# Kernel optimization log

Measured on AMD Instinct MI355X. Metric: run time of the kernel, lower is better.

## Reference

```python
import jax, jax.numpy as jnp
import numpy as np

K = 3          # kernel_size
PAD = 1        # padding
HEADS = 4
C = 128
K2 = K * K


def setup_inputs() -> dict:
    key = jax.random.key(0)
    k1, k2, k3, k4 = jax.random.split(key, 4)
    B, H, W = 4, 128, 128
    x = jax.random.normal(k1, (B, H, W, C), jnp.float32)
    w_qkv = jax.random.normal(k2, (K2 * K2 * HEADS, C), jnp.float32) * 0.02
    w_v = jax.random.normal(k3, (K2, C, C), jnp.float32) * np.sqrt(2.0 / (K2 * C))
    w_proj = jax.random.normal(k4, (C, C), jnp.float32) * 0.02
    return {"x": x, "w_qkv": w_qkv, "w_v": w_v, "w_proj": w_proj}


def _csa(x, w_qkv, w_v, w_proj):
    B, H, W, Cc = x.shape
    hd = Cc // HEADS
    scale = hd ** (-0.5)
    N = H * W
    # attention map: Linear(C -> k^4*heads); pool is identity for stride=1
    att = jnp.einsum('bhwc,oc->bhwo', x, w_qkv)                      # [B,H,W,81*heads]
    att = att.reshape(B, N, HEADS, K2, K2).transpose(0, 2, 1, 3, 4)  # [B,heads,N,k2,k2]
    att = jax.nn.softmax(att * scale, axis=-1)
    # unfold x into per-location 3x3 windows (patch index p = di*K + dj)
    xp = jnp.pad(x, ((0, 0), (PAD, PAD), (PAD, PAD), (0, 0)))
    patches = jnp.stack([xp[:, di:di + H, dj:dj + W, :]
                         for di in range(K) for dj in range(K)], axis=3)  # [B,H,W,k2,C]
    v = patches.reshape(B, N, K2, Cc)
    # grouped 1x1 conv == per-window-position CxC matmul
    v = jnp.einsum('pij,bnpj->bnpi', w_v, v)                          # [B,N,k2,C]
    v = v.reshape(B, N, K2, HEADS, hd).transpose(0, 3, 1, 2, 4)       # [B,heads,N,k2,hd]
    out = jnp.einsum('bhnpq,bhnqd->bhnpd', att, v)                    # [B,heads,N,k2,hd]
    # -> [B, C, k2, H, W] with channel index = head*hd + d (matches torch fold layout)
    out = out.transpose(0, 1, 4, 3, 2).reshape(B, Cc, K2, H, W)
    # fold: scatter-add overlapping patches back to (H, W)
    acc = jnp.zeros((B, Cc, H + 2 * PAD, W + 2 * PAD), x.dtype)
    p = 0
    for di in range(K):
        for dj in range(K):
            acc = acc.at[:, :, di:di + H, dj:dj + W].add(out[:, :, p])
            p += 1
    y = acc[:, :, PAD:PAD + H, PAD:PAD + W].transpose(0, 2, 3, 1)     # [B,H,W,C]
    return jnp.einsum('bhwc,oc->bhwo', y, w_proj)


def reference(x, w_qkv, w_v, w_proj):
    return _csa(x, w_qkv, w_v, w_proj)
```

## Files before the change

kernel.cpp:

```cpp
#include <hip/hip_runtime.h>


typedef short bf16x8 __attribute__((ext_vector_type(8)));
typedef float f32x4  __attribute__((ext_vector_type(4)));
typedef float v2f    __attribute__((ext_vector_type(2)));

#define SCALE 0.17677669529663687f

__device__ __forceinline__ unsigned short f2bf(float f) {
  unsigned u = __float_as_uint(f);
  u = (u + 0x7fffu + ((u >> 16) & 1u)) >> 16;
  return (unsigned short)u;
}
__device__ __forceinline__ float bf2f(unsigned short s) {
  return __uint_as_float(((unsigned)s) << 16);
}
__device__ __forceinline__ unsigned pk2bf(float lo, float hi) {
  unsigned a = __float_as_uint(lo) + 0x8000u;
  unsigned b = __float_as_uint(hi) + 0x8000u;
  return __builtin_amdgcn_perm(b, a, 0x07060302u);
}
__device__ __forceinline__ bf16x8 ld16(const unsigned short* p) {
  union { bf16x8 v; uint4 u; } r;
  r.u = *(const uint4*)p;
  return r.v;
}

__global__ __launch_bounds__(256) void cvt_kernel(const float* __restrict__ wq,
                                                  const float* __restrict__ wv,
                                                  const float* __restrict__ wp,
                                                  unsigned short* __restrict__ wqb,
                                                  unsigned short* __restrict__ wvb2,
                                                  unsigned short* __restrict__ wpb2) {
  int i = blockIdx.x * 256 + threadIdx.x;
  if (i >= 30848) return;
  if (i < 10368) {
    long off = (long)i * 4;
    float4 v = *(const float4*)(wq + off);
    ushort4 o;
    o.x = f2bf(v.x); o.y = f2bf(v.y); o.z = f2bf(v.z); o.w = f2bf(v.w);
    *(ushort4*)(wqb + off) = o;
    return;
  }
  const float* s;
  unsigned short* d;
  if (i < 28800) {
    int it = i - 10368;
    int l = it & 63, mk = it >> 6;
    int kk = mk & 3, m = (mk >> 2) & 1, qcg = mk >> 3;
    int cg = qcg & 3, q = qcg >> 2;
    int chan = cg * 32 + m * 16 + (l & 15);
    int k0 = kk * 32 + (l >> 4) * 8;
    s = wv + (long)q * 16384 + chan * 128 + k0;
    d = wvb2 + (long)it * 8;
  } else {
    int it = i - 28800;
    int l = it & 63, kk = (it >> 6) & 3, tn = it >> 8;
    int col = tn * 16 + (l & 15);
    int k0 = kk * 32 + (l >> 4) * 8;
    s = wp + (long)col * 128 + k0;
    d = wpb2 + (long)it * 8;
  }
  float4 a = *(const float4*)s, b = *(const float4*)(s + 4);
  ushort4 o0, o1;
  o0.x = f2bf(a.x); o0.y = f2bf(a.y); o0.z = f2bf(a.z); o0.w = f2bf(a.w);
  o1.x = f2bf(b.x); o1.y = f2bf(b.y); o1.z = f2bf(b.z); o1.w = f2bf(b.w);
  *(ushort4*)d = o0;
  *(ushort4*)(d + 4) = o1;
}

__device__ __forceinline__ void softmax9(const float* L, unsigned short* attile,
                                         int row, int p) {
  float mx = L[0];
#pragma unroll
  for (int q = 1; q < 9; q++) mx = fmaxf(mx, L[q]);
  float e[9], s = 0.f;
#pragma unroll
  for (int q = 0; q < 9; q++) { e[q] = __expf((L[q] - mx) * SCALE); s += e[q]; }
  float inv = 1.f / s;
#pragma unroll
  for (int q = 0; q < 9; q++) attile[row * 90 + q * 10 + p] = f2bf(e[q] * inv);
}

__global__ __launch_bounds__(512, 6) void att_kernel(const float* __restrict__ x,
                                                     const unsigned short* __restrict__ wqb,
                                                     unsigned* __restrict__ attb) {
  __shared__ unsigned short Bl[96 * 136];
  __shared__ float lg[64][84];
  const int t = threadIdx.x;
  const long m0 = (long)blockIdx.x * 64;
  const int w = t >> 6, lane = t & 63, qd = lane >> 4, l15 = lane & 15;
  const int rw = w & 3, th = w >> 2;
  const int sr0 = t / 9, sp0 = t - sr0 * 9;
  const int sr1 = (t + 512) / 9, sp1 = (t + 512) - sr1 * 9;
  int dsto[6], srco[6];
#pragma unroll
  for (int k = 0; k < 6; k++) {
    int i = t + k * 512;
    if (i < 2880) {
      int q = i / 320, rem = i - q * 320, n = rem / 5, j = rem - n * 5;
      dsto[k] = (int)(((size_t)(q * 4) * 65536 + m0 + n) * 5 + j);
      srco[k] = n * 45 + q * 5 + j;
    } else { dsto[k] = -1; srco[k] = 0; }
  }
  bf16x8 af[4];
  {
    const float* xr = x + (m0 + rw * 16 + l15) * 128 + qd * 8;
#pragma unroll
    for (int kk = 0; kk < 4; kk++) {
      float4 a = *(const float4*)(xr + kk * 32);
      float4 b = *(const float4*)(xr + kk * 32 + 4);
      union { uint4 u; bf16x8 v; } r;
      r.u = make_uint4(pk2bf(a.x, a.y), pk2bf(a.z, a.w),
                       pk2bf(b.x, b.y), pk2bf(b.z, b.w));
      af[kk] = r.v;
    }
  }
  unsigned short* attile = Bl;
  for (int h = 0; h < 4; h++) {
    __syncthreads();
#pragma unroll
    for (int k = 0; k < 3; k++) {
      int i = t + k * 512;
      if (i < 1296) {
        int row = i >> 4, seg = i & 15;
        const uint4 v = *(const uint4*)(wqb + (long)(h * 81 + row) * 128 + seg * 8);
        *(uint4*)((unsigned*)Bl + row * 68 + seg * 4) = v;
      }
    }
    __syncthreads();
    f32x4 acc[3] = {};
#pragma unroll
    for (int kk = 0; kk < 4; kk++)
#pragma unroll
      for (int tn = 0; tn < 3; tn++) {
        bf16x8 bf = ld16(Bl + ((th * 3 + tn) * 16 + l15) * 136 + kk * 32 + qd * 8);
        acc[tn] = __builtin_amdgcn_mfma_f32_16x16x32_bf16(af[kk], bf, acc[tn], 0, 0, 0);
      }
#pragma unroll
    for (int tn = 0; tn < 3; tn++)
#pragma unroll
      for (int r = 0; r < 4; r++) {
        int col = (th * 3 + tn) * 16 + l15;
        if (col < 81) lg[rw * 16 + qd * 4 + r][col] = acc[tn][r];
      }
    __syncthreads();
    softmax9(&lg[sr0][sp0 * 9], attile, sr0, sp0);
    if (t < 64) softmax9(&lg[sr1][sp1 * 9], attile, sr1, sp1);
    __syncthreads();
#pragma unroll
    for (int k = 0; k < 6; k++)
      if (dsto[k] >= 0)
        attb[dsto[k] + h * 327680] = ((const unsigned*)attile)[srco[k]];
  }
}

__global__ __launch_bounds__(512, 4) void av_kernel(const float* __restrict__ x,
                                                    const unsigned short* __restrict__ wvb2,
                                                    const unsigned* __restrict__ attb,
                                                    const unsigned short* __restrict__ wpb2,
                                                    float* __restrict__ out) {
  __shared__ unsigned short A[144 * 136];
  __shared__ unsigned short S[100 * 136];
  __shared__ unsigned aLs[2400];
  const int t = threadIdx.x;
  const int bb = blockIdx.z;
  const int r0 = blockIdx.y * 8, c0 = blockIdx.x * 8;
  const int l15 = t & 15, qd = (t >> 4) & 3, wvi = t >> 6;
  const int lane = t & 63;
  const int cg = wvi & 3, lp = wvi >> 2;
  const int n = (wvi & 3) * 16 + l15, lr = n >> 3, lc = n & 7;
  const int g = (wvi >> 2) * 4 + qd, head = g >> 1;
  const long nb = (long)bb * 16384;
  unsigned* Sdw = (unsigned*)S;
  unsigned* Adw = (unsigned*)A;

  int xbI[4];
#pragma unroll
  for (int i = 0; i < 4; i++) {
    int tile = lp * 4 + i;
    int ml = tile < 7 ? tile * 16 + l15 : 0;
    xbI[i] = (ml / 10) * 12 + (ml % 10) + 13;
  }

#pragma unroll
  for (int k = 0; k < 9; k++) {
    int i = t + k * 512;
    int row = i >> 5, seg = i & 31;
    int gr = r0 - 2 + row / 12, gc = c0 - 2 + row % 12;
    float4 v = make_float4(0.f, 0.f, 0.f, 0.f);
    if (gr >= 0 && gr < 128 && gc >= 0 && gc < 128)
      v = *(const float4*)(x + (nb + gr * 128 + gc) * 128 + seg * 4);
    *(uint2*)(Adw + row * 68 + seg * 2) = make_uint2(pk2bf(v.x, v.y), pk2bf(v.z, v.w));
  }

  int aoff[4], aidx[4];
#pragma unroll
  for (int k = 0; k < 4; k++) {
    int i = t + k * 512;
    if (i < 2000) {
      int hh = i / 500, rem = i - hh * 500, row = rem / 5, j5 = rem - row * 5;
      int gr = r0 - 1 + row / 10, gc = c0 - 1 + row % 10;
      aidx[k] = hh * 600 + row * 6 + j5;
      aoff[k] = (gr >= 0 && gr < 128 && gc >= 0 && gc < 128)
                    ? (int)(((size_t)hh * 65536 + nb + gr * 128 + gc) * 5 + j5)
                    : -1;
    } else { aidx[k] = -1; aoff[k] = -1; }
  }
  const unsigned short* pwv = wvb2 + cg * 4096 + lane * 8;

  v2f y2[8];
#pragma unroll
  for (int i = 0; i < 8; i++) y2[i] = (v2f){0.f, 0.f};

  unsigned avv[4];
  bf16x8 wvf[2][4];

#define LOAD_A(qq)                                                              \
  { _Pragma("unroll") for (int k = 0; k < 4; k++)                               \
      avv[k] = (aoff[k] >= 0) ? attb[aoff[k] + (qq) * 1310720] : 0u; }
#define LOAD_WV(qq)                                                             \
  { _Pragma("unroll") for (int m = 0; m < 2; m++)                               \
    _Pragma("unroll") for (int kk = 0; kk < 4; kk++)                            \
      wvf[m][kk] = *(const bf16x8*)(pwv + (size_t)(qq) * 16384 +                \
                                    (m * 4 + kk) * 512); }

  LOAD_A(0)
  LOAD_WV(0)

  for (int q = 0; q < 9; q++) {
    const int qoff = (q / 3) * 12 + (q % 3) - 13;
    __syncthreads();

#pragma unroll
    for (int k = 0; k < 4; k++)
      if (aidx[k] >= 0) aLs[aidx[k]] = avv[k];

#pragma unroll
    for (int i = 0; i < 4; i++) {
      const int tile = lp * 4 + i;
      if (tile < 7) {
        int xr = xbI[i] + qoff;
        xr = xr > 143 ? 143 : xr;
        bf16x8 bx[4];
#pragma unroll
        for (int kk = 0; kk < 4; kk++)
          bx[kk] = ld16(A + xr * 136 + kk * 32 + qd * 8);
        f32x4 acc[2];
#pragma unroll
        for (int m = 0; m < 2; m++) acc[m] = (f32x4){0.f, 0.f, 0.f, 0.f};
#pragma unroll
        for (int kk = 0; kk < 4; kk++)
#pragma unroll
          for (int m = 0; m < 2; m++)
            acc[m] = __builtin_amdgcn_mfma_f32_16x16x32_bf16(wvf[m][kk], bx[kk],
                                                             acc[m], 0, 0, 0);
        int loc = tile * 16 + l15;
        if (loc < 100) {
#pragma unroll
          for (int m = 0; m < 2; m++)
            *(uint2*)(Sdw + loc * 68 + cg * 16 + m * 8 + qd * 2) =
                make_uint2(pk2bf(acc[m][0], acc[m][1]),
                           pk2bf(acc[m][2], acc[m][3]));
        }
      }
    }
    __syncthreads();
    if (q < 8) { LOAD_A(q + 1) LOAD_WV(q + 1) }

    const unsigned short* aS = (const unsigned short*)aLs;
    const int mlb = lr * 10 + lc + 11;
#pragma unroll
    for (int p = 0; p < 9; p++) {
      const int ml = mlb + (1 - p / 3) * 10 + (1 - p % 3);
      const float a = bf2f(aS[head * 1200 + ml * 12 + p]);
      const v2f a2 = {a, a};
      const uint4* Sr = (const uint4*)(Sdw + ml * 68 + g * 8);
#pragma unroll
      for (int v4 = 0; v4 < 2; v4++) {
        const uint4 u = Sr[v4];
        v2f xv;
        const int yi = v4 * 4;
        xv.x = __uint_as_float(u.x << 16); xv.y = __uint_as_float(u.x & 0xffff0000u);
        y2[yi + 0] += a2 * xv;
        xv.x = __uint_as_float(u.y << 16); xv.y = __uint_as_float(u.y & 0xffff0000u);
        y2[yi + 1] += a2 * xv;
        xv.x = __uint_as_float(u.z << 16); xv.y = __uint_as_float(u.z & 0xffff0000u);
        y2[yi + 2] += a2 * xv;
        xv.x = __uint_as_float(u.w << 16); xv.y = __uint_as_float(u.w & 0xffff0000u);
        y2[yi + 3] += a2 * xv;
      }
    }
  }

  __syncthreads();
  unsigned short* yb = A;
  {
    uint4 pk[2];
#pragma unroll
    for (int v4 = 0; v4 < 2; v4++) {
      pk[v4].x = pk2bf(y2[v4 * 4 + 0].x, y2[v4 * 4 + 0].y);
      pk[v4].y = pk2bf(y2[v4 * 4 + 1].x, y2[v4 * 4 + 1].y);
      pk[v4].z = pk2bf(y2[v4 * 4 + 2].x, y2[v4 * 4 + 2].y);
      pk[v4].w = pk2bf(y2[v4 * 4 + 3].x, y2[v4 * 4 + 3].y);
    }
    uint4* dst = (uint4*)(Adw + n * 68 + g * 8);
    dst[0] = pk[0]; dst[1] = pk[1];
  }
  __syncthreads();
  f32x4 pacc[4] = {};
#pragma unroll
  for (int kk = 0; kk < 4; kk++) {
    bf16x8 afr = ld16(yb + ((wvi & 3) * 16 + l15) * 136 + kk * 32 + qd * 8);
#pragma unroll
    for (int tn = 0; tn < 4; tn++) {
      bf16x8 bfr = *(const bf16x8*)(wpb2 + (((wvi >> 2) * 4 + tn) * 4 + kk) * 512 +
                                    lane * 8);
      pacc[tn] = __builtin_amdgcn_mfma_f32_16x16x32_bf16(afr, bfr, pacc[tn], 0, 0, 0);
    }
  }
#pragma unroll
  for (int tn = 0; tn < 4; tn++)
#pragma unroll
    for (int r = 0; r < 4; r++) {
      int nl = (wvi & 3) * 16 + qd * 4 + r;
      int col = ((wvi >> 2) * 4 + tn) * 16 + l15;
      out[(nb + (r0 + (nl >> 3)) * 128 + (c0 + (nl & 7))) * 128 + col] = pacc[tn][r];
    }
}

extern "C" void kernel_launch(void* const* d_in, const int* in_sizes, int n_in,
                              void* d_out, int out_size, void* d_ws, size_t ws_size,
                              hipStream_t stream) {
  const float* x  = (const float*)d_in[0];
  const float* wq = (const float*)d_in[1];
  const float* wv = (const float*)d_in[2];
  const float* wp = (const float*)d_in[3];
  char* w = (char*)d_ws;
  unsigned*       attb = (unsigned*)w;
  unsigned short* wqb  = (unsigned short*)(w + 47185920);
  unsigned short* wvb2 = wqb + 41472;
  unsigned short* wpb2 = wvb2 + 147456;

  cvt_kernel<<<121, 256, 0, stream>>>(wq, wv, wp, wqb, wvb2, wpb2);
  att_kernel<<<1024, 512, 0, stream>>>(x, wqb, attb);
  dim3 g3(16, 16, 4);
  av_kernel<<<g3, 512, 0, stream>>>(x, wvb2, attb, wpb2, (float*)d_out);
}
```

Before: 191.1 us.

## Move softmax from attention-logit kernel into AV kernel, store raw bf16 logits

```diff
diff --git a/kernel.cpp b/kernel.cpp
--- a/kernel.cpp
+++ b/kernel.cpp
@@ -69,30 +69,15 @@
   *(ushort4*)(d + 4) = o1;
 }
 
-__device__ __forceinline__ void softmax9(const float* L, unsigned short* attile,
-                                         int row, int p) {
-  float mx = L[0];
-#pragma unroll
-  for (int q = 1; q < 9; q++) mx = fmaxf(mx, L[q]);
-  float e[9], s = 0.f;
-#pragma unroll
-  for (int q = 0; q < 9; q++) { e[q] = __expf((L[q] - mx) * SCALE); s += e[q]; }
-  float inv = 1.f / s;
-#pragma unroll
-  for (int q = 0; q < 9; q++) attile[row * 90 + q * 10 + p] = f2bf(e[q] * inv);
-}
-
-__global__ __launch_bounds__(512, 6) void att_kernel(const float* __restrict__ x,
+__global__ __launch_bounds__(512, 4) void att_kernel(const float* __restrict__ x,
                                                      const unsigned short* __restrict__ wqb,
-                                                     unsigned* __restrict__ attb) {
+                                                     unsigned* __restrict__ lgb) {
   __shared__ unsigned short Bl[96 * 136];
-  __shared__ float lg[64][84];
+  __shared__ unsigned short attile[5760];
   const int t = threadIdx.x;
   const long m0 = (long)blockIdx.x * 64;
   const int w = t >> 6, lane = t & 63, qd = lane >> 4, l15 = lane & 15;
   const int rw = w & 3, th = w >> 2;
-  const int sr0 = t / 9, sp0 = t - sr0 * 9;
-  const int sr1 = (t + 512) / 9, sp1 = (t + 512) - sr1 * 9;
   int dsto[6], srco[6];
 #pragma unroll
   for (int k = 0; k < 6; k++) {
@@ -103,6 +88,14 @@
       srco[k] = n * 45 + q * 5 + j;
     } else { dsto[k] = -1; srco[k] = 0; }
   }
+  int ati[3]; bool ok[3];
+#pragma unroll
+  for (int tn = 0; tn < 3; tn++) {
+    int c = th * 48 + tn * 16 + l15;
+    ok[tn] = c < 81;
+    int p = c / 9, q9 = c - p * 9;
+    ati[tn] = (rw * 16 + qd * 4) * 90 + q9 * 10 + p;
+  }
   bf16x8 af[4];
   {
     const float* xr = x + (m0 + rw * 16 + l15) * 128 + qd * 8;
@@ -116,19 +109,22 @@
       af[kk] = r.v;
     }
   }
-  unsigned short* attile = Bl;
+  unsigned* ATdw = (unsigned*)attile;
+
+#define STAGE_BL(hh)                                                            \
+  { _Pragma("unroll") for (int k = 0; k < 3; k++) {                             \
+      int i = t + k * 512;                                                      \
+      if (i < 1296) {                                                           \
+        int row = i >> 4, seg = i & 15;                                         \
+        const uint4 v = *(const uint4*)(wqb + (long)((hh) * 81 + row) * 128 +   \
+                                        seg * 8);                               \
+        *(uint4*)((unsigned*)Bl + row * 68 + seg * 4) = v;                      \
+      }                                                                         \
+    } }
+
+  STAGE_BL(0)
+  __syncthreads();
   for (int h = 0; h < 4; h++) {
-    __syncthreads();
-#pragma unroll
-    for (int k = 0; k < 3; k++) {
-      int i = t + k * 512;
-      if (i < 1296) {
-        int row = i >> 4, seg = i & 15;
-        const uint4 v = *(const uint4*)(wqb + (long)(h * 81 + row) * 128 + seg * 8);
-        *(uint4*)((unsigned*)Bl + row * 68 + seg * 4) = v;
-      }
-    }
-    __syncthreads();
     f32x4 acc[3] = {};
 #pragma unroll
     for (int kk = 0; kk < 4; kk++)
@@ -139,25 +135,23 @@
       }
 #pragma unroll
     for (int tn = 0; tn < 3; tn++)
-#pragma unroll
-      for (int r = 0; r < 4; r++) {
-        int col = (th * 3 + tn) * 16 + l15;
-        if (col < 81) lg[rw * 16 + qd * 4 + r][col] = acc[tn][r];
-      }
+      if (ok[tn])
+#pragma unroll
+        for (int r = 0; r < 4; r++)
+          attile[ati[tn] + r * 90] = f2bf(acc[tn][r]);
     __syncthreads();
-    softmax9(&lg[sr0][sp0 * 9], attile, sr0, sp0);
-    if (t < 64) softmax9(&lg[sr1][sp1 * 9], attile, sr1, sp1);
-    __syncthreads();
+    if (h < 3) STAGE_BL(h + 1)
 #pragma unroll
     for (int k = 0; k < 6; k++)
       if (dsto[k] >= 0)
-        attb[dsto[k] + h * 327680] = ((const unsigned*)attile)[srco[k]];
+        lgb[dsto[k] + h * 327680] = ATdw[srco[k]];
+    __syncthreads();
   }
 }
 
 __global__ __launch_bounds__(512, 4) void av_kernel(const float* __restrict__ x,
                                                     const unsigned short* __restrict__ wvb2,
-                                                    const unsigned* __restrict__ attb,
+                                                    const unsigned* __restrict__ lgb,
                                                     const unsigned short* __restrict__ wpb2,
                                                     float* __restrict__ out) {
   __shared__ unsigned short A[144 * 136];
@@ -183,17 +177,6 @@
     xbI[i] = (ml / 10) * 12 + (ml % 10) + 13;
   }
 
-#pragma unroll
-  for (int k = 0; k < 9; k++) {
-    int i = t + k * 512;
-    int row = i >> 5, seg = i & 31;
-    int gr = r0 - 2 + row / 12, gc = c0 - 2 + row % 12;
-    float4 v = make_float4(0.f, 0.f, 0.f, 0.f);
-    if (gr >= 0 && gr < 128 && gc >= 0 && gc < 128)
-      v = *(const float4*)(x + (nb + gr * 128 + gc) * 128 + seg * 4);
-    *(uint2*)(Adw + row * 68 + seg * 2) = make_uint2(pk2bf(v.x, v.y), pk2bf(v.z, v.w));
-  }
-
   int aoff[4], aidx[4];
 #pragma unroll
   for (int k = 0; k < 4; k++) {
@@ -207,6 +190,31 @@
                     : -1;
     } else { aidx[k] = -1; aoff[k] = -1; }
   }
+
+  float is0[4], is1[4];
+#pragma unroll
+  for (int k = 0; k < 4; k++) {
+    float s0 = 0.f, s1 = 0.f;
+#pragma unroll
+    for (int q9 = 0; q9 < 9; q9++) {
+      unsigned dv = (aoff[k] >= 0) ? lgb[aoff[k] + q9 * 1310720] : 0u;
+      s0 += __expf(__uint_as_float(dv << 16) * SCALE);
+      s1 += __expf(__uint_as_float(dv & 0xffff0000u) * SCALE);
+    }
+    is0[k] = 1.f / s0; is1[k] = 1.f / s1;
+  }
+
+#pragma unroll
+  for (int k = 0; k < 9; k++) {
+    int i = t + k * 512;
+    int row = i >> 5, seg = i & 31;
+    int gr = r0 - 2 + row / 12, gc = c0 - 2 + row % 12;
+    float4 v = make_float4(0.f, 0.f, 0.f, 0.f);
+    if (gr >= 0 && gr < 128 && gc >= 0 && gc < 128)
+      v = *(const float4*)(x + (nb + gr * 128 + gc) * 128 + seg * 4);
+    *(uint2*)(Adw + row * 68 + seg * 2) = make_uint2(pk2bf(v.x, v.y), pk2bf(v.z, v.w));
+  }
+
   const unsigned short* pwv = wvb2 + cg * 4096 + lane * 8;
 
   v2f y2[8];
@@ -218,7 +226,7 @@
 
 #define LOAD_A(qq)                                                              \
   { _Pragma("unroll") for (int k = 0; k < 4; k++)                               \
-      avv[k] = (aoff[k] >= 0) ? attb[aoff[k] + (qq) * 1310720] : 0u; }
+      avv[k] = (aoff[k] >= 0) ? lgb[aoff[k] + (qq) * 1310720] : 0u; }
 #define LOAD_WV(qq)                                                             \
   { _Pragma("unroll") for (int m = 0; m < 2; m++)                               \
     _Pragma("unroll") for (int kk = 0; kk < 4; kk++)                            \
@@ -234,7 +242,16 @@
 
 #pragma unroll
     for (int k = 0; k < 4; k++)
-      if (aidx[k] >= 0) aLs[aidx[k]] = avv[k];
+      if (aidx[k] >= 0) {
+        unsigned pv = 0;
+        if (aoff[k] >= 0) {
+          unsigned dv = avv[k];
+          float plo = __expf(__uint_as_float(dv << 16) * SCALE) * is0[k];
+          float phi = __expf(__uint_as_float(dv & 0xffff0000u) * SCALE) * is1[k];
+          pv = pk2bf(plo, phi);
+        }
+        aLs[aidx[k]] = pv;
+      }
 
 #pragma unroll
     for (int i = 0; i < 4; i++) {
@@ -337,13 +354,13 @@
   const float* wv = (const float*)d_in[2];
   const float* wp = (const float*)d_in[3];
   char* w = (char*)d_ws;
-  unsigned*       attb = (unsigned*)w;
+  unsigned*       lgb  = (unsigned*)w;
   unsigned short* wqb  = (unsigned short*)(w + 47185920);
   unsigned short* wvb2 = wqb + 41472;
   unsigned short* wpb2 = wvb2 + 147456;
 
   cvt_kernel<<<121, 256, 0, stream>>>(wq, wv, wp, wqb, wvb2, wpb2);
-  att_kernel<<<1024, 512, 0, stream>>>(x, wqb, attb);
+  att_kernel<<<1024, 512, 0, stream>>>(x, wqb, lgb);
   dim3 g3(16, 16, 4);
-  av_kernel<<<g3, 512, 0, stream>>>(x, wvb2, attb, wpb2, (float*)d_out);
-}
+  av_kernel<<<g3, 512, 0, stream>>>(x, wvb2, lgb, wpb2, (float*)d_out);
+}
```

New measurement: 205.9 us. +7.8%, slower.
